# Performance work log

Hardware: AMD Instinct MI355X
Metric: run time of the kernel (lower is better)

Reference implementation:

```python
import jax, jax.numpy as jnp
import numpy as np

H = 512        # edge_feature_size (input_size == hidden_size)
B = 8          # batch
N = 8192       # n_nodes


def setup_inputs() -> dict:
    key = jax.random.key(0)
    k1, k2, k3, k4 = jax.random.split(key, 4)
    # Glorot-ish init scale like torch GRU (uniform +-1/sqrt(H))
    s = 1.0 / np.sqrt(H)
    e_wv = jax.random.normal(k1, (B, H, N), dtype=jnp.float32)
    m_wv = jax.random.normal(k2, (B, H, N), dtype=jnp.float32)
    # torch GRU weight layout: [3H, H] stacked as (reset, update, new)
    W_ih = jax.random.uniform(k3, (3 * H, H), dtype=jnp.float32, minval=-s, maxval=s)
    W_hh = jax.random.uniform(k4, (3 * H, H), dtype=jnp.float32, minval=-s, maxval=s)
    return {"e_wv": e_wv, "m_wv": m_wv, "W_ih": W_ih, "W_hh": W_hh}


def reference(e_wv, m_wv, W_ih, W_hh):
    # Single-step GRU cell (no bias), applied to all nodes at once.
    # e_wv: hidden state h0 [B, H, N]; m_wv: input x [B, H, N].
    gi = jnp.einsum('gh,bhn->bgn', W_ih, m_wv)   # [B, 3H, N]
    gh = jnp.einsum('gh,bhn->bgn', W_hh, e_wv)   # [B, 3H, N]
    i_r, i_z, i_n = gi[:, :H], gi[:, H:2 * H], gi[:, 2 * H:]
    h_r, h_z, h_n = gh[:, :H], gh[:, H:2 * H], gh[:, 2 * H:]
    r = jax.nn.sigmoid(i_r + h_r)
    z = jax.nn.sigmoid(i_z + h_z)
    n = jnp.tanh(i_n + r * h_n)
    return (1.0 - z) * n + z * e_wv              # [B, H, N]
```

## Files before the change

### kernel.cpp

```cpp
#include <hip/hip_runtime.h>
#include <hip/hip_bf16.h>


#define HH 512
#define NBATCH 8
#define NN 8192
#define BN 128
#define BK 64
#define NSTEPS 16
#define THREADS 256
#define A_BYTES (192 * BK * 2)
#define B_BYTES (BN * BK * 2)
#define BUF_BYTES (A_BYTES + B_BYTES)
#define LDS_TOTAL (2 * BUF_BYTES)

typedef __attribute__((ext_vector_type(8))) short short8;
typedef __attribute__((ext_vector_type(4))) float f32x4;

__device__ __forceinline__ unsigned cvt_pk_bf16(float a, float b) {
  unsigned r;
  asm("v_cvt_pk_bf16_f32 %0, %1, %2" : "=v"(r) : "v"(a), "v"(b));
  return r;
}

__device__ __forceinline__ void gload_lds16(const void* g, void* l) {
  __builtin_amdgcn_global_load_lds(
      (__attribute__((address_space(1))) void*)(g),
      (__attribute__((address_space(3))) void*)(l), 16, 0, 0);
}

#define MFMA16(a_, b_, c_) __builtin_amdgcn_mfma_f32_16x16x32_bf16((a_), (b_), (c_), 0, 0, 0)

__global__ void prepack_w(const float* __restrict__ W_ih, const float* __restrict__ W_hh,
                          __hip_bfloat16* __restrict__ ws) {
  int t = blockIdx.x * 256 + threadIdx.x;
  int blk = t / 12288;
  int e = t % 12288;
  int ra = e >> 6;
  int kk = (e & 63) ^ ((ra & 7) << 3);
  int gate = ra >> 6;
  int h = (blk >> 4) * 64 + (ra & 63);
  int row = gate * HH + h;
  int kg = (blk & 15) * 64 + kk;
  float v = (kg < 512) ? W_ih[row * 512 + kg] : W_hh[row * 512 + (kg - 512)];
  ws[t] = __float2bfloat16(v);
}

__global__ __launch_bounds__(THREADS, 2)
void gru_main(const float* __restrict__ e_wv, const float* __restrict__ m_wv,
              const __hip_bfloat16* __restrict__ wimg, float* __restrict__ out) {
  extern __shared__ char smem[];
  const int tid  = threadIdx.x;
  const int lane = tid & 63;
  const int wave = tid >> 6;
  const int wm = wave >> 1;
  const int wn = wave & 1;

  const int wg  = blockIdx.x;
  const int swz = (wg & 7) * 512 + (wg >> 3);
  const int ht  = swz & 7;
  const int nt  = (swz >> 3) & 63;
  const int b   = swz >> 9;

  const int k0  = (tid & 15) << 2;
  const int n0s = (tid >> 4) << 3;

  const size_t batch_off = (size_t)b * HH * NN;
  const float* xm = m_wv + batch_off + (size_t)k0 * NN + nt * BN + n0s;
  const float* xe = e_wv + batch_off + (size_t)k0 * NN + nt * BN + n0s;
  const char*  wA = (const char*)wimg + (size_t)ht * NSTEPS * A_BYTES + tid * 16;

  f32x4 acc_r[2][4]  = {};
  f32x4 acc_z[2][4]  = {};
  f32x4 acc_in[2][4] = {};
  f32x4 acc_hn[2][4] = {};

  int aoff[2], boff[2];
#pragma unroll
  for (int kb2 = 0; kb2 < 2; ++kb2) {
    const int ke2 = kb2 * 64 + ((lane >> 4) << 4);
    const int sw  = (lane & 7) << 4;
    aoff[kb2] = (wm * 32 + (lane & 15)) * 128 + (ke2 ^ sw);
    boff[kb2] = A_BYTES + (wn * 64 + (lane & 15)) * 128 + (ke2 ^ sw);
  }

  auto issue_A = [&](int s, char* nb) {
    const char* gA = wA + (size_t)s * A_BYTES;
    char* lA = nb + tid * 16;
#pragma unroll
    for (int i = 0; i < 6; ++i)
      gload_lds16(gA + i * 4096, lA + i * 4096);
  };
  auto x_load_half = [&](const float* xs, int h, f32x4 c[4]) {
#pragma unroll
    for (int i = 0; i < 4; ++i) c[i] = *(const f32x4*)(xs + (size_t)i * NN + h * 4);
  };
  auto x_write_half = [&](char* nb, int h, const f32x4 c[4]) {
    char* Bb = nb + A_BYTES;
#pragma unroll
    for (int j2 = 0; j2 < 4; ++j2) {
      const int j = h * 4 + j2;
      unsigned lo = cvt_pk_bf16(c[0][j2], c[1][j2]);
      unsigned hi = cvt_pk_bf16(c[2][j2], c[3][j2]);
      int off = (n0s + j) * 128 + ((k0 * 2) ^ (j << 4));
      *(uint2*)(Bb + off) = make_uint2(lo, hi);
    }
  };
  auto compute_kb2 = [&](const char* cb, int kb2, bool firstHalf) {
    short8 bfr[4];
#pragma unroll
    for (int ni = 0; ni < 4; ++ni)
      bfr[ni] = *(const short8*)(cb + boff[kb2] + ni * 2048);
    {
      short8 a0 = *(const short8*)(cb + aoff[kb2]);
      short8 a1 = *(const short8*)(cb + aoff[kb2] + 2048);
#pragma unroll
      for (int ni = 0; ni < 4; ++ni) {
        acc_r[0][ni] = MFMA16(a0, bfr[ni], acc_r[0][ni]);
        acc_r[1][ni] = MFMA16(a1, bfr[ni], acc_r[1][ni]);
      }
    }
    {
      short8 a0 = *(const short8*)(cb + aoff[kb2] + 8192);
      short8 a1 = *(const short8*)(cb + aoff[kb2] + 8192 + 2048);
#pragma unroll
      for (int ni = 0; ni < 4; ++ni) {
        acc_z[0][ni] = MFMA16(a0, bfr[ni], acc_z[0][ni]);
        acc_z[1][ni] = MFMA16(a1, bfr[ni], acc_z[1][ni]);
      }
    }
    {
      short8 a0 = *(const short8*)(cb + aoff[kb2] + 16384);
      short8 a1 = *(const short8*)(cb + aoff[kb2] + 16384 + 2048);
      if (firstHalf) {
#pragma unroll
        for (int ni = 0; ni < 4; ++ni) {
          acc_in[0][ni] = MFMA16(a0, bfr[ni], acc_in[0][ni]);
          acc_in[1][ni] = MFMA16(a1, bfr[ni], acc_in[1][ni]);
        }
      } else {
#pragma unroll
        for (int ni = 0; ni < 4; ++ni) {
          acc_hn[0][ni] = MFMA16(a0, bfr[ni], acc_hn[0][ni]);
          acc_hn[1][ni] = MFMA16(a1, bfr[ni], acc_hn[1][ni]);
        }
      }
    }
  };

  issue_A(0, smem);
  {
    f32x4 c[4];
    x_load_half(xm, 0, c);
    x_write_half(smem, 0, c);
    x_load_half(xm, 1, c);
    x_write_half(smem, 1, c);
  }
  __syncthreads();

#pragma unroll 1
  for (int s = 0; s < NSTEPS; ++s) {
    char* cb = smem + ((s & 1) ? BUF_BYTES : 0);
    char* nb = smem + ((s & 1) ? 0 : BUF_BYTES);
    const bool pre = (s < NSTEPS - 1);
    const bool firstHalf = (s < 8);
    const float* xs = (s + 1 < 8 ? xm : xe) + (size_t)((s + 1) & 7) * (64 * NN);

    f32x4 c[4];
    if (pre) x_load_half(xs, 0, c);
    if (pre) issue_A(s + 1, nb);
    compute_kb2(cb, 0, firstHalf);
    if (pre) { x_write_half(nb, 0, c); x_load_half(xs, 1, c); }
    compute_kb2(cb, 1, firstHalf);
    if (pre) x_write_half(nb, 1, c);
    __syncthreads();
  }

  const size_t obase = batch_off + (size_t)(ht * 64 + wm * 32) * NN + nt * BN + wn * 64;
  const float* ep = e_wv + obase;
  float* op = out + obase;
  const int rsub = (lane >> 4) << 2;
  const int csub = lane & 15;
#pragma unroll
  for (int mi = 0; mi < 2; ++mi)
#pragma unroll
    for (int ni = 0; ni < 4; ++ni) {
#pragma unroll
      for (int r = 0; r < 4; ++r) {
        size_t idx = (size_t)(mi * 16 + rsub + r) * NN + ni * 16 + csub;
        float pr  = acc_r[mi][ni][r];
        float pz  = acc_z[mi][ni][r];
        float vin = acc_in[mi][ni][r];
        float vhn = acc_hn[mi][ni][r];
        float rr  = 1.f / (1.f + __expf(-pr));
        float zz  = 1.f / (1.f + __expf(-pz));
        float ex  = __expf(2.f * (vin + rr * vhn));
        float nn2 = 1.f - 2.f / (ex + 1.f);
        float ev  = ep[idx];
        op[idx] = (1.f - zz) * nn2 + zz * ev;
      }
    }
}

extern "C" void kernel_launch(void* const* d_in, const int* in_sizes, int n_in,
                              void* d_out, int out_size, void* d_ws, size_t ws_size,
                              hipStream_t stream) {
  const float* e_wv = (const float*)d_in[0];
  const float* m_wv = (const float*)d_in[1];
  const float* W_ih = (const float*)d_in[2];
  const float* W_hh = (const float*)d_in[3];
  float* out = (float*)d_out;
  __hip_bfloat16* wimg = (__hip_bfloat16*)d_ws;

  (void)hipFuncSetAttribute((const void*)gru_main,
                            hipFuncAttributeMaxDynamicSharedMemorySize, LDS_TOTAL);

  prepack_w<<<(NBATCH * NSTEPS * 12288) / 256, 256, 0, stream>>>(W_ih, W_hh, wimg);
  gru_main<<<NBATCH * 8 * 64, THREADS, LDS_TOTAL, stream>>>(e_wv, m_wv, wimg, out);
}
```

Before: 385.0 us.

## Restructure X tile loading to coalesced float2 rows with full-step prefetch and setprio

Changes how the activation tile is staged: each wave now loads 16 K-rows as float2 per lane (coalesced across N), holds the full step in registers, and writes 16-byte packed bf16 vectors to LDS with a new swizzle that matches the updated B-fragment read offsets. The whole next step's X load is issued before compute, and the write is deferred until after both MFMA halves, giving more latency hiding. It also raises wave priority around the MFMA section. This costs 32 extra VGPRs for prefetched data, which may pressure occupancy at 2 blocks per CU.

Result: faster. 317.2 us (-17.6%).

```diff
diff --git a/kernel.cpp b/kernel.cpp
--- a/kernel.cpp
+++ b/kernel.cpp
@@ -10,7 +10,7 @@
 #define NSTEPS 16
 #define THREADS 256
 #define A_BYTES (192 * BK * 2)
-#define B_BYTES (BN * BK * 2)
+#define B_BYTES (BN * 128)
 #define BUF_BYTES (A_BYTES + B_BYTES)
 #define LDS_TOTAL (2 * BUF_BYTES)
 
@@ -62,26 +62,24 @@
   const int nt  = (swz >> 3) & 63;
   const int b   = swz >> 9;
 
-  const int k0  = (tid & 15) << 2;
-  const int n0s = (tid >> 4) << 3;
-
   const size_t batch_off = (size_t)b * HH * NN;
-  const float* xm = m_wv + batch_off + (size_t)k0 * NN + nt * BN + n0s;
-  const float* xe = e_wv + batch_off + (size_t)k0 * NN + nt * BN + n0s;
+  const float* xm = m_wv + batch_off + (size_t)(16 * wave) * NN + nt * BN + 2 * lane;
+  const float* xe = e_wv + batch_off + (size_t)(16 * wave) * NN + nt * BN + 2 * lane;
   const char*  wA = (const char*)wimg + (size_t)ht * NSTEPS * A_BYTES + tid * 16;
 
   f32x4 acc_r[2][4]  = {};
   f32x4 acc_z[2][4]  = {};
   f32x4 acc_in[2][4] = {};
   f32x4 acc_hn[2][4] = {};
+  float2 xR[16];
 
   int aoff[2], boff[2];
 #pragma unroll
   for (int kb2 = 0; kb2 < 2; ++kb2) {
-    const int ke2 = kb2 * 64 + ((lane >> 4) << 4);
-    const int sw  = (lane & 7) << 4;
-    aoff[kb2] = (wm * 32 + (lane & 15)) * 128 + (ke2 ^ sw);
-    boff[kb2] = A_BYTES + (wn * 64 + (lane & 15)) * 128 + (ke2 ^ sw);
+    const int K = kb2 * 64 + ((lane >> 4) << 4);
+    aoff[kb2] = (wm * 32 + (lane & 15)) * 128 + (K ^ ((lane & 7) << 4));
+    boff[kb2] = A_BYTES + (wn * 64 + (lane & 15)) * 128
+              + (K ^ (((lane >> 1) & 7) << 4));
   }
 
   auto issue_A = [&](int s, char* nb) {
@@ -91,19 +89,28 @@
     for (int i = 0; i < 6; ++i)
       gload_lds16(gA + i * 4096, lA + i * 4096);
   };
-  auto x_load_half = [&](const float* xs, int h, f32x4 c[4]) {
-#pragma unroll
-    for (int i = 0; i < 4; ++i) c[i] = *(const f32x4*)(xs + (size_t)i * NN + h * 4);
-  };
-  auto x_write_half = [&](char* nb, int h, const f32x4 c[4]) {
-    char* Bb = nb + A_BYTES;
-#pragma unroll
-    for (int j2 = 0; j2 < 4; ++j2) {
-      const int j = h * 4 + j2;
-      unsigned lo = cvt_pk_bf16(c[0][j2], c[1][j2]);
-      unsigned hi = cvt_pk_bf16(c[2][j2], c[3][j2]);
-      int off = (n0s + j) * 128 + ((k0 * 2) ^ (j << 4));
-      *(uint2*)(Bb + off) = make_uint2(lo, hi);
+  auto x_load = [&](const float* xs) {
+#pragma unroll
+    for (int i = 0; i < 16; ++i)
+      xR[i] = *(const float2*)(xs + (size_t)i * NN);
+  };
+  auto write_X = [&](char* nb) {
+    char* Bb = nb + A_BYTES + (2 * lane) * 128;
+    const int sx = (lane & 7) << 4;
+#pragma unroll
+    for (int o = 0; o < 2; ++o) {
+      uint4 w0, w1;
+      w0.x = cvt_pk_bf16(xR[8 * o + 0].x, xR[8 * o + 1].x);
+      w0.y = cvt_pk_bf16(xR[8 * o + 2].x, xR[8 * o + 3].x);
+      w0.z = cvt_pk_bf16(xR[8 * o + 4].x, xR[8 * o + 5].x);
+      w0.w = cvt_pk_bf16(xR[8 * o + 6].x, xR[8 * o + 7].x);
+      w1.x = cvt_pk_bf16(xR[8 * o + 0].y, xR[8 * o + 1].y);
+      w1.y = cvt_pk_bf16(xR[8 * o + 2].y, xR[8 * o + 3].y);
+      w1.z = cvt_pk_bf16(xR[8 * o + 4].y, xR[8 * o + 5].y);
+      w1.w = cvt_pk_bf16(xR[8 * o + 6].y, xR[8 * o + 7].y);
+      const int kb = (32 * wave + 16 * o) ^ sx;
+      *(uint4*)(Bb + kb)       = w0;
+      *(uint4*)(Bb + 128 + kb) = w1;
     }
   };
   auto compute_kb2 = [&](const char* cb, int kb2, bool firstHalf) {
@@ -149,13 +156,8 @@
   };
 
   issue_A(0, smem);
-  {
-    f32x4 c[4];
-    x_load_half(xm, 0, c);
-    x_write_half(smem, 0, c);
-    x_load_half(xm, 1, c);
-    x_write_half(smem, 1, c);
-  }
+  x_load(xm);
+  write_X(smem);
   __syncthreads();
 
 #pragma unroll 1
@@ -164,15 +166,17 @@
     char* nb = smem + ((s & 1) ? 0 : BUF_BYTES);
     const bool pre = (s < NSTEPS - 1);
     const bool firstHalf = (s < 8);
-    const float* xs = (s + 1 < 8 ? xm : xe) + (size_t)((s + 1) & 7) * (64 * NN);
-
-    f32x4 c[4];
-    if (pre) x_load_half(xs, 0, c);
-    if (pre) issue_A(s + 1, nb);
+
+    if (pre) {
+      const int t = s + 1;
+      x_load((t < 8 ? xm : xe) + (size_t)(t & 7) * (64 * NN));
+      issue_A(t, nb);
+    }
+    __builtin_amdgcn_s_setprio(1);
     compute_kb2(cb, 0, firstHalf);
-    if (pre) { x_write_half(nb, 0, c); x_load_half(xs, 1, c); }
     compute_kb2(cb, 1, firstHalf);
-    if (pre) x_write_half(nb, 1, c);
+    __builtin_amdgcn_s_setprio(0);
+    if (pre) write_X(nb);
     __syncthreads();
   }
 
```
